# Kernel tuning notes

Hardware: AMD Instinct MI355X
Metric: run time of the kernel (lower is better)

## Reference

```python
import jax, jax.numpy as jnp
import numpy as np

N = 8192


def setup_inputs() -> dict:
    key = jax.random.key(0)
    k1, k2, k3 = jax.random.split(key, 3)
    # valid xyxy boxes: x1y1 in [0,1000), wh in (0,100]
    xy = jax.random.uniform(k1, (N, 2), dtype=jnp.float32) * 1000.0
    wh = jax.random.uniform(k2, (N, 2), dtype=jnp.float32) * 100.0 + 1.0
    boxes = jnp.concatenate([xy, xy + wh], axis=-1)  # [N,4]
    scores = jax.random.uniform(k3, (N,), dtype=jnp.float32)
    return {"boxes": boxes, "scores": scores, "iou_threshold": 0.5, "max_outputs": 100}


def _nms_keep_flags(boxes_sorted, iou_threshold):
    # boxes_sorted: [N,4] in descending-score order
    x1, y1, x2, y2 = (boxes_sorted[:, i] for i in range(4))
    areas = (x2 - x1) * (y2 - y1)  # [N]
    # pairwise intersection [N,N]
    iw = jnp.maximum(jnp.minimum(x2[:, None], x2[None, :]) - jnp.maximum(x1[:, None], x1[None, :]), 0.0)
    ih = jnp.maximum(jnp.minimum(y2[:, None], y2[None, :]) - jnp.maximum(y1[:, None], y1[None, :]), 0.0)
    inter = iw * ih
    iou = inter / (areas[:, None] + areas[None, :] - inter)
    sup = iou > iou_threshold  # [N,N]; diagonal True but handled below

    def body(suppressed, row):
        sup_row, i = row
        keep_i = jnp.logical_not(suppressed[i])
        suppressed = jnp.where(keep_i, suppressed | sup_row, suppressed)
        return suppressed, keep_i

    _, keep_flags = jax.lax.scan(
        body, jnp.zeros(sup.shape[0], dtype=bool), (sup, jnp.arange(sup.shape[0]))
    )
    return keep_flags  # [N] bool, in sorted order


def reference(boxes, scores, iou_threshold, max_outputs):
    n = scores.shape[0]
    order = jnp.argsort(-scores)  # descending, stable (matches torch sort tie-break)
    keep_flags = _nms_keep_flags(boxes[order], iou_threshold)
    # positions (in sorted order) of kept boxes; non-kept pushed to end
    pos = jnp.where(keep_flags, jnp.arange(n), n)
    pos = jnp.sort(pos)[:max_outputs]
    valid = pos < n
    idx = order[jnp.minimum(pos, n - 1)]
    # pad with -1 beyond the number of kept boxes (fixed-shape stand-in for keep[:max_outputs])
    return jnp.where(valid, idx, -1).astype(jnp.int32)
```

## Files before the change

kernel.cpp:

```cpp
#include <hip/hip_runtime.h>
#include <stdint.h>

#define THREADS 1024
#define NWAVE 16
#define NB 1024
#define NH 16
#define CAP 256
#define WANT 128
#define MAXKEEP 128
#define T0 0.9765625f

__device__ __forceinline__ float fence(float x) {
  asm("" : "+v"(x));
  return x;
}

__device__ __forceinline__ uint32_t rdlane32(uint32_t v, int l) {
  return (uint32_t)__builtin_amdgcn_readlane((int)v, l);
}

#define REGSTAGE(KK, JV)                                              \
  do {                                                                \
    _Pragma("unroll") for (int v = 0; v < 4; ++v) {                   \
      if ((v & (JV)) == 0) {                                          \
        uint64_t a = k[v], b = k[v | (JV)];                           \
        bool descRun = (((v * 64) & (KK)) == 0);                      \
        uint64_t mx = a > b ? a : b, mn = a > b ? b : a;              \
        k[v] = descRun ? mx : mn;                                     \
        k[v | (JV)] = descRun ? mn : mx;                              \
      }                                                               \
    }                                                                 \
  } while (0)

#define SHSTAGE(KK, J)                                                \
  do {                                                                \
    _Pragma("unroll") for (int v = 0; v < 4; ++v) {                   \
      uint64_t a = k[v];                                              \
      uint64_t b = __shfl_xor(a, (J), 64);                            \
      int e = v * 64 + lane;                                          \
      bool descRun = ((e & (KK)) == 0);                               \
      bool lower = ((lane & (J)) == 0);                               \
      uint64_t mx = a > b ? a : b, mn = a > b ? b : a;                \
      k[v] = (descRun == lower) ? mx : mn;                            \
    }                                                                 \
  } while (0)

#define SH32TO1(KK)                                                   \
  SHSTAGE(KK, 32); SHSTAGE(KK, 16); SHSTAGE(KK, 8);                   \
  SHSTAGE(KK, 4); SHSTAGE(KK, 2); SHSTAGE(KK, 1)

__device__ __forceinline__ void sort256(int lane, int cnt,
                                        const uint64_t* cand, uint64_t k[4]) {
#pragma unroll
  for (int v = 0; v < 4; ++v) {
    int e = v * 64 + lane;
    k[v] = (e < cnt) ? cand[e] : 0ull;
  }
  SHSTAGE(2, 1);
  SHSTAGE(4, 2); SHSTAGE(4, 1);
  SHSTAGE(8, 4); SHSTAGE(8, 2); SHSTAGE(8, 1);
  SHSTAGE(16, 8); SHSTAGE(16, 4); SHSTAGE(16, 2); SHSTAGE(16, 1);
  SHSTAGE(32, 16); SHSTAGE(32, 8); SHSTAGE(32, 4); SHSTAGE(32, 2);
  SHSTAGE(32, 1);
  SHSTAGE(64, 32); SHSTAGE(64, 16); SHSTAGE(64, 8); SHSTAGE(64, 4);
  SHSTAGE(64, 2); SHSTAGE(64, 1);
  REGSTAGE(128, 1); SH32TO1(128);
  REGSTAGE(256, 2); REGSTAGE(256, 1); SH32TO1(256);
}

__device__ __forceinline__ int greedy4(int lane, int cnt, int kept, int maxout,
                                       float thr, const uint64_t k[4],
                                       const float4* candbox, float4* cbox,
                                       float* careaS, float4* kbox,
                                       float* kareaS, int* kidxS) {
#pragma unroll
  for (int c = 0; c < 4; ++c) {
    if (c * 64 < cnt && kept < maxout) {
      uint64_t key = k[c];
      bool valid = (c * 64 + lane) < cnt;
      int slot = valid ? (int)(key & 0x3FFFF) : 0;
      int idx = valid ? (8192 - (int)((key >> 18) & 0x3FFF)) : 0;
      float4 bb = candbox[slot];
      float x1 = bb.x, y1 = bb.y, x2 = bb.z, y2 = bb.w;
      float areaj = fence((x2 - x1) * (y2 - y1));
      const int kbase = kept;

      bool supp = !valid;
#pragma unroll 4
      for (int t = 0; t < kbase; ++t) {
        float4 kb = kbox[t];
        float ka = kareaS[t];
        float iw = fmaxf(fminf(kb.z, x2) - fmaxf(kb.x, x1), 0.0f);
        float ih = fmaxf(fminf(kb.w, y2) - fmaxf(kb.y, y1), 0.0f);
        float inter = fence(iw * ih);
        float denom = (ka + areaj) - inter;
        if (inter / denom > thr) supp = true;
      }

      cbox[lane] = bb;
      careaS[lane] = areaj;
      uint64_t row = 0;
#pragma unroll 8
      for (int j = 0; j < 64; ++j) {
        float4 ib = cbox[j];
        float ia = careaS[j];
        float iw = fmaxf(fminf(ib.z, x2) - fmaxf(ib.x, x1), 0.0f);
        float ih = fmaxf(fminf(ib.w, y2) - fmaxf(ib.y, y1), 0.0f);
        float inter = fence(iw * ih);
        float denom = (ia + areaj) - inter;
        if (inter / denom > thr) row |= (1ull << j);
      }

      const uint64_t self = 1ull << lane;
      uint64_t alive = __ballot(valid && !supp);
      uint64_t rowNS = row & ~self;
      uint64_t conflict = __ballot(valid && !supp && ((rowNS & alive) != 0));
      uint64_t keepm;
      const int budget = maxout - kept;
      if (conflict == 0) {
        int na = __popcll((unsigned long long)alive);
        if (na <= budget) {
          keepm = alive;
          kept += na;
        } else {
          int lo = 0;
#pragma unroll
          for (int s = 32; s >= 1; s >>= 1) {
            int t2 = lo + s;
            uint64_t mk = (t2 >= 64) ? ~0ull : ((1ull << t2) - 1ull);
            if (__popcll((unsigned long long)(alive & mk)) < budget) lo = t2;
          }
          uint64_t mk2 = ((lo + 1) >= 64) ? ~0ull : ((1ull << (lo + 1)) - 1ull);
          keepm = alive & mk2;
          kept += budget;
        }
      } else {
        uint32_t rlo = (uint32_t)row, rhi = (uint32_t)(row >> 32);
        keepm = 0;
        while (alive != 0 && kept < maxout) {
          int b2 = __ffsll((unsigned long long)alive) - 1;
          keepm |= (1ull << b2);
          kept++;
          uint64_t rb = ((uint64_t)rdlane32(rhi, b2) << 32) |
                        (uint64_t)rdlane32(rlo, b2);
          alive &= ~rb;
          alive &= ~(1ull << b2);
        }
      }
      if ((keepm >> lane) & 1) {
        int rank = __popcll((unsigned long long)(keepm & (self - 1ull)));
        kbox[kbase + rank] = bb;
        kareaS[kbase + rank] = areaj;
        kidxS[kbase + rank] = idx;
      }
    }
  }
  return kept;
}

__global__ __launch_bounds__(THREADS) void nms_rank4_kernel(
    const float* __restrict__ boxes, const float* __restrict__ scores, int n,
    const float* __restrict__ thr_p, const int* __restrict__ maxout_p,
    int* __restrict__ out, int out_size) {
  __shared__ __align__(16) uint32_t hist[NH][NB];
  __shared__ uint32_t wcnt[NWAVE];
  __shared__ uint64_t cand[CAP];
  __shared__ float4 candbox[CAP];
  __shared__ float4 candboxR[CAP];
  __shared__ float2 cxyR[CAP];
  __shared__ float areaR[CAP];
  __shared__ int sidxR[CAP];
  __shared__ uint64_t adjm[CAP][4];
  __shared__ float4 cbox[64];
  __shared__ float careaS[64];
  __shared__ float4 kbox[MAXKEEP];
  __shared__ float kareaS[MAXKEEP];
  __shared__ int kidxS[MAXKEEP];
  __shared__ int s_cut, s_hi, s_kept, s_done;

  const int tid = threadIdx.x;
  const int lane = tid & 63;
  const int wid = tid >> 6;

  const float thr = *thr_p;
  int maxout = *maxout_p;
  if (maxout > out_size) maxout = out_size;
  if (maxout > MAXKEEP) maxout = MAXKEEP;

  float sc[8];
  const int base = tid * 8;
  if (base + 7 < n) {
    const float4* sp = reinterpret_cast<const float4*>(scores) + 2 * tid;
    float4 a = sp[0], b2 = sp[1];
    sc[0] = a.x; sc[1] = a.y; sc[2] = a.z; sc[3] = a.w;
    sc[4] = b2.x; sc[5] = b2.y; sc[6] = b2.z; sc[7] = b2.w;
  } else {
#pragma unroll
    for (int r = 0; r < 8; ++r)
      sc[r] = (base + r < n) ? scores[base + r] : -1.0f;
  }

  int wtot = 0;
#pragma unroll
  for (int r = 0; r < 8; ++r) {
    bool pred = (base + r < n) && (sc[r] >= T0);
    wtot += __popcll((unsigned long long)__ballot(pred));
  }
  if (lane == 0) wcnt[wid] = (uint32_t)wtot;
  __syncthreads();
  int cbase = 0, total = 0;
#pragma unroll
  for (int w = 0; w < NWAVE; ++w) {
    int c = (int)wcnt[w];
    if (w < wid) cbase += c;
    total += c;
  }

  const bool fast_ok = (total <= CAP);
  bool done = false;
  if (fast_ok) {
    int run = cbase;
#pragma unroll
    for (int r = 0; r < 8; ++r) {
      int idx = base + r;
      bool pred = (idx < n) && (sc[r] >= T0);
      uint64_t m = __ballot(pred);
      if (pred) {
        int pos = run + __popcll((unsigned long long)(m & ((1ull << lane) - 1)));
        cand[pos] = ((uint64_t)__float_as_uint(sc[r]) << 32) |
                    ((uint64_t)(8192 - idx) << 18) | (uint64_t)pos;
      }
      run += __popcll((unsigned long long)m);
    }
    if (tid >= total && tid < CAP) cand[tid] = 0;
    __syncthreads();

    const int cnt = total;
    const int c = tid >> 2;
    const int h = tid & 3;

    uint64_t mykey = 0;
    float4 bb;
    int myidx = 0;
    if (c < cnt) {
      mykey = cand[c];
      if (h == 0) {
        myidx = 8192 - (int)((mykey >> 18) & 0x3FFF);
        bb = *reinterpret_cast<const float4*>(boxes + 4 * (size_t)myidx);
      }
    }

    int rc = 0;
    {
      int r0 = 0, r1 = 0;
#pragma unroll
      for (int i = 0; i < CAP / 8; ++i) {
        uint64_t ka = cand[8 * i + h];
        uint64_t kb = cand[8 * i + 4 + h];
        r0 += (ka > mykey) ? 1 : 0;
        r1 += (kb > mykey) ? 1 : 0;
      }
      rc = r0 + r1;
    }
    rc += __shfl_xor(rc, 1, 64);
    rc += __shfl_xor(rc, 2, 64);
    if (c < cnt && h == 0) {
      candboxR[rc] = bb;
      sidxR[rc] = myidx;
      cxyR[rc] = make_float2((bb.x + bb.z) * 0.5f, (bb.y + bb.w) * 0.5f);
      areaR[rc] = fence((bb.z - bb.x) * (bb.w - bb.y));
    }
    __syncthreads();

    if (c < cnt) {
      float4 mb = candboxR[c];
      float marea = areaR[c];
      float mcx = (mb.x + mb.z) * 0.5f;
      float mcy = (mb.y + mb.w) * 0.5f;
      float mrx = (mb.z - mb.x) * 0.5f;
      float mry = (mb.w - mb.y) * 0.5f;
      const bool use_pf = (thr >= 0.0f);
      uint64_t acc = 0;
      const int qbase = h << 6;
#pragma unroll
      for (int j = 0; j < 64; ++j) {
        const int q = qbase + j;
        if (q < cnt) {
          float2 cq = cxyR[q];
          float2 eq = make_float2(candboxR[q].z - candboxR[q].x,
                                  candboxR[q].w - candboxR[q].y);
          float dx = fabsf(cq.x - mcx);
          float dy = fabsf(cq.y - mcy);
          bool close = !use_pf | ((dx * 2.0f <= (mrx * 2.0f + eq.x) * 1.0000002f) &
                                  (dy * 2.0f <= (mry * 2.0f + eq.y) * 1.0000002f));
          if (close) {
            float4 qb = candboxR[q];
            float qarea = areaR[q];
            float iw = fmaxf(fminf(qb.z, mb.z) - fmaxf(qb.x, mb.x), 0.0f);
            float ih = fmaxf(fminf(qb.w, mb.w) - fmaxf(qb.y, mb.y), 0.0f);
            float inter = fence(iw * ih);
            float denom = (qarea + marea) - inter;
            if (inter / denom > thr) acc |= (1ull << j);
          }
        }
      }
      adjm[c][h] = acc;
    }
    __syncthreads();

    if (wid == 0) {
      uint64_t km[4] = {0, 0, 0, 0};
      int kept = 0;
#pragma unroll
      for (int cch = 0; cch < 4; ++cch) {
        if (cch * 64 < cnt && kept < maxout) {
          const int p = cch * 64 + lane;
          const bool valid = p < cnt;
          uint64_t r0 = 0, r1 = 0, r2 = 0, r3 = 0;
          if (valid) {
            r0 = adjm[p][0]; r1 = adjm[p][1];
            r2 = adjm[p][2]; r3 = adjm[p][3];
          }
          const uint64_t self = 1ull << lane;
          bool supp = !valid ||
                      (((r0 & km[0]) | (r1 & km[1]) | (r2 & km[2]) |
                        (r3 & km[3])) != 0);
          uint64_t alive = __ballot(valid && !supp);
          uint64_t wc = (cch == 0) ? r0 : (cch == 1) ? r1 : (cch == 2) ? r2 : r3;
          uint64_t conflict =
              __ballot(valid && !supp && ((wc & ~self & alive) != 0));
          uint64_t keepm;
          const int kbase = kept;
          const int budget = maxout - kept;
          if (conflict == 0) {
            int na = __popcll((unsigned long long)alive);
            if (na <= budget) {
              keepm = alive;
              kept += na;
            } else {
              int lo = 0;
#pragma unroll
              for (int s = 32; s >= 1; s >>= 1) {
                int t2 = lo + s;
                uint64_t mk = (t2 >= 64) ? ~0ull : ((1ull << t2) - 1ull);
                if (__popcll((unsigned long long)(alive & mk)) < budget) lo = t2;
              }
              uint64_t mk2 =
                  ((lo + 1) >= 64) ? ~0ull : ((1ull << (lo + 1)) - 1ull);
              keepm = alive & mk2;
              kept += budget;
            }
          } else {
            uint32_t rlo = (uint32_t)wc, rhi = (uint32_t)(wc >> 32);
            keepm = 0;
            while (alive != 0 && kept < maxout) {
              int b2 = __ffsll((unsigned long long)alive) - 1;
              keepm |= (1ull << b2);
              kept++;
              uint64_t rb = ((uint64_t)rdlane32(rhi, b2) << 32) |
                            (uint64_t)rdlane32(rlo, b2);
              alive &= ~rb;
              alive &= ~(1ull << b2);
            }
          }
          km[cch] = keepm;
          if ((keepm >> lane) & 1) {
            int rk = kbase +
                     __popcll((unsigned long long)(keepm & (self - 1ull)));
            kidxS[rk] = sidxR[p];
            float4 pb = candboxR[p];
            kbox[rk] = pb;
            kareaS[rk] = fence((pb.z - pb.x) * (pb.w - pb.y));
          }
        }
      }
      if (lane == 0) {
        s_kept = kept;
        s_done = (kept >= maxout) ? 1 : 0;
      }
    }
    __syncthreads();
    done = (s_done != 0);
  }

  if (!done) {
    {
      uint32_t* hh = &hist[0][0];
      for (int i = tid; i < NH * NB; i += THREADS) hh[i] = 0;
    }
    if (tid == 0) {
      s_hi = fast_ok ? 999 : (NB - 1);
      if (!fast_ok) s_kept = 0;
      s_done = 0;
    }
    __syncthreads();
    const int hicap = fast_ok ? 999 : (NB - 1);
    {
      uint32_t* myh = hist[wid];
#pragma unroll
      for (int r = 0; r < 8; ++r) {
        if (base + r < n) {
          int b = (int)(sc[r] * (float)NB);
          b = b < 0 ? 0 : (b > NB - 1 ? NB - 1 : b);
          if (b <= hicap) atomicAdd(&myh[b], 1u);
        }
      }
    }
    __syncthreads();
    for (int i = tid; i < NB; i += THREADS) {
      uint32_t s = 0;
#pragma unroll
      for (int hh = 0; hh < NH; ++hh) s += hist[hh][i];
      hist[0][i] = s;
    }
    __syncthreads();

    while (true) {
      if (wid == 0) {
        uint32_t csum = 0;
        const uint4* hp = reinterpret_cast<const uint4*>(&hist[0][lane * 16]);
#pragma unroll
        for (int i = 0; i < 4; ++i) {
          uint4 h4 = hp[i];
          csum += h4.x + h4.y + h4.z + h4.w;
        }
        uint32_t suf = csum;
#pragma unroll
        for (int off = 1; off < 64; off <<= 1) {
          uint32_t v = __shfl_down(suf, off, 64);
          suf += (lane + off < 64) ? v : 0u;
        }
        uint64_t mask = __ballot(suf >= (uint32_t)WANT);
        int cut;
        if (mask == 0) {
          cut = 0;
        } else {
          int cstar = 63 - __builtin_clzll((unsigned long long)mask);
          int src = cstar + 1 < 63 ? cstar + 1 : 63;
          uint32_t above_raw = __shfl(suf, src, 64);
          uint32_t above = (cstar < 63) ? above_raw : 0u;
          uint32_t h2 = (lane < 16) ? hist[0][cstar * 16 + lane] : 0u;
          uint32_t suf2 = h2;
#pragma unroll
          for (int off = 1; off < 64; off <<= 1) {
            uint32_t v = __shfl_down(suf2, off, 64);
            suf2 += (lane + off < 64) ? v : 0u;
          }
          uint64_t mask2 =
              __ballot((lane < 16) && (above + suf2 >= (uint32_t)WANT));
          int b2 = 63 - __builtin_clzll((unsigned long long)mask2);
          cut = cstar * 16 + b2;
        }
        if (lane == 0) s_cut = cut;
      }
      __syncthreads();
      const int cut = s_cut;
      const int hi = s_hi;
      const float lo_f =
          (cut == 0) ? -__builtin_huge_valf() : (float)cut / (float)NB;
      const bool top_open = (hi == NB - 1);
      const float up_f = (float)(hi + 1) / (float)NB;

      int wt = 0;
#pragma unroll
      for (int r = 0; r < 8; ++r) {
        int idx = base + r;
        bool pred = (idx < n) && (sc[r] >= lo_f) && (top_open || sc[r] < up_f);
        wt += __popcll((unsigned long long)__ballot(pred));
      }
      if (lane == 0) wcnt[wid] = (uint32_t)wt;
      __syncthreads();
      int cb2 = 0, tot2 = 0;
#pragma unroll
      for (int w = 0; w < NWAVE; ++w) {
        int cc = (int)wcnt[w];
        if (w < wid) cb2 += cc;
        tot2 += cc;
      }
      {
        int run2 = cb2;
#pragma unroll
        for (int r = 0; r < 8; ++r) {
          int idx = base + r;
          bool pred =
              (idx < n) && (sc[r] >= lo_f) && (top_open || sc[r] < up_f);
          uint64_t m = __ballot(pred);
          if (pred) {
            int pos =
                run2 + __popcll((unsigned long long)(m & ((1ull << lane) - 1)));
            if (pos < CAP) {
              cand[pos] = ((uint64_t)__float_as_uint(sc[r]) << 32) |
                          ((uint64_t)(8192 - idx) << 18) | (uint64_t)pos;
              candbox[pos] =
                  *reinterpret_cast<const float4*>(boxes + 4 * (size_t)idx);
            }
          }
          run2 += __popcll((unsigned long long)m);
        }
      }
      __syncthreads();
      int cnt2 = tot2 > CAP ? CAP : tot2;
      if (wid == 0) {
        uint64_t k2[4];
        sort256(lane, cnt2, cand, k2);
        int kept = greedy4(lane, cnt2, s_kept, maxout, thr, k2, candbox, cbox,
                           careaS, kbox, kareaS, kidxS);
        if (lane == 0) {
          s_kept = kept;
          s_hi = cut - 1;
          s_done = (kept >= maxout || cut == 0) ? 1 : 0;
        }
      }
      __syncthreads();
      if (s_done) break;
      for (int b = cut + tid; b <= hi; b += THREADS) hist[0][b] = 0;
      __syncthreads();
    }
  }

  const int keptf = s_kept;
  for (int i = tid; i < out_size; i += THREADS)
    out[i] = (i < keptf) ? kidxS[i] : -1;
}

extern "C" void kernel_launch(void* const* d_in, const int* in_sizes, int n_in,
                              void* d_out, int out_size, void* d_ws,
                              size_t ws_size, hipStream_t stream) {
  const float* boxes = (const float*)d_in[0];
  const float* scores = (const float*)d_in[1];
  const float* thr = (const float*)d_in[2];
  const int* maxout = (const int*)d_in[3];
  int n = in_sizes[1];
  int* out = (int*)d_out;

  hipLaunchKernelGGL(nms_rank4_kernel, dim3(1), dim3(THREADS), 0, stream,
                     boxes, scores, n, thr, maxout, out, out_size);
}
```

Baseline: 26.16 us.

## Redistribute IoU rows across threads, use max-radius prefilter, batch greedy conflict resolution

Remaps the adjacency computation so each thread handles one (candidate, 64-column chunk) pair by tid&255 and tid>>8, skipping chunks beyond the candidate count. It replaces the per-pair proximity test with a cheaper bound built from a block-wide max half-extent reduced through shuffles and an LDS atomicMax. The greedy pass now keeps whole conflict-free runs at once and only falls back to one step per conflicting lane, then trims to the output budget. Wave 0 also writes the output directly and the block returns early, so the final global store is skipped. This adds a reduction, an atomic and a looser prefilter that may admit more exact IoU checks.

```diff
diff --git a/kernel.cpp b/kernel.cpp
--- a/kernel.cpp
+++ b/kernel.cpp
@@ -158,7 +158,7 @@
   return kept;
 }
 
-__global__ __launch_bounds__(THREADS) void nms_rank4_kernel(
+__global__ __launch_bounds__(THREADS) void nms_rank5_kernel(
     const float* __restrict__ boxes, const float* __restrict__ scores, int n,
     const float* __restrict__ thr_p, const int* __restrict__ maxout_p,
     int* __restrict__ out, int out_size) {
@@ -176,7 +176,7 @@
   __shared__ float4 kbox[MAXKEEP];
   __shared__ float kareaS[MAXKEEP];
   __shared__ int kidxS[MAXKEEP];
-  __shared__ int s_cut, s_hi, s_kept, s_done;
+  __shared__ int s_cut, s_hi, s_kept, s_done, s_rmax_i;
 
   const int tid = threadIdx.x;
   const int lane = tid & 63;
@@ -207,6 +207,7 @@
     wtot += __popcll((unsigned long long)__ballot(pred));
   }
   if (lane == 0) wcnt[wid] = (uint32_t)wtot;
+  if (tid == 0) s_rmax_i = 0;
   __syncthreads();
   int cbase = 0, total = 0;
 #pragma unroll
@@ -264,6 +265,15 @@
     }
     rc += __shfl_xor(rc, 1, 64);
     rc += __shfl_xor(rc, 2, 64);
+
+    float rm = 0.0f;
+    if (c < cnt && h == 0)
+      rm = fmaxf((bb.z - bb.x) * 0.5f, (bb.w - bb.y) * 0.5f);
+#pragma unroll
+    for (int off = 1; off < 64; off <<= 1)
+      rm = fmaxf(rm, __shfl_xor(rm, off, 64));
+    if (lane == 0) atomicMax(&s_rmax_i, __float_as_int(rm));
+
     if (c < cnt && h == 0) {
       candboxR[rc] = bb;
       sidxR[rc] = myidx;
@@ -272,39 +282,45 @@
     }
     __syncthreads();
 
-    if (c < cnt) {
-      float4 mb = candboxR[c];
-      float marea = areaR[c];
-      float mcx = (mb.x + mb.z) * 0.5f;
-      float mcy = (mb.y + mb.w) * 0.5f;
-      float mrx = (mb.z - mb.x) * 0.5f;
-      float mry = (mb.w - mb.y) * 0.5f;
-      const bool use_pf = (thr >= 0.0f);
-      uint64_t acc = 0;
-      const int qbase = h << 6;
-#pragma unroll
-      for (int j = 0; j < 64; ++j) {
-        const int q = qbase + j;
-        if (q < cnt) {
-          float2 cq = cxyR[q];
-          float2 eq = make_float2(candboxR[q].z - candboxR[q].x,
-                                  candboxR[q].w - candboxR[q].y);
-          float dx = fabsf(cq.x - mcx);
-          float dy = fabsf(cq.y - mcy);
-          bool close = !use_pf | ((dx * 2.0f <= (mrx * 2.0f + eq.x) * 1.0000002f) &
-                                  (dy * 2.0f <= (mry * 2.0f + eq.y) * 1.0000002f));
-          if (close) {
-            float4 qb = candboxR[q];
-            float qarea = areaR[q];
-            float iw = fmaxf(fminf(qb.z, mb.z) - fmaxf(qb.x, mb.x), 0.0f);
-            float ih = fmaxf(fminf(qb.w, mb.w) - fmaxf(qb.y, mb.y), 0.0f);
-            float inter = fence(iw * ih);
-            float denom = (qarea + marea) - inter;
-            if (inter / denom > thr) acc |= (1ull << j);
-          }
-        }
-      }
-      adjm[c][h] = acc;
+    {
+      const int c2 = tid & 255;
+      const int h2 = tid >> 8;
+      const int qbase = h2 << 6;
+      if (c2 < cnt) {
+        uint64_t acc = 0;
+        if (qbase < cnt) {
+          float4 mb = candboxR[c2];
+          float marea = areaR[c2];
+          float mcx = (mb.x + mb.z) * 0.5f;
+          float mcy = (mb.y + mb.w) * 0.5f;
+          float mrx = (mb.z - mb.x) * 0.5f;
+          float mry = (mb.w - mb.y) * 0.5f;
+          const float rmaxf = __int_as_float(s_rmax_i);
+          const float limx = mrx + rmaxf + 0.002f;
+          const float limy = mry + rmaxf + 0.002f;
+          const bool use_pf = (thr >= 0.0f);
+#pragma unroll
+          for (int j = 0; j < 64; ++j) {
+            const int q = qbase + j;
+            if (q < cnt) {
+              float2 cq = cxyR[q];
+              bool close = (fabsf(cq.x - mcx) <= limx) &
+                           (fabsf(cq.y - mcy) <= limy);
+              if (!use_pf) close = true;
+              if (close) {
+                float4 qb = candboxR[q];
+                float qarea = areaR[q];
+                float iw = fmaxf(fminf(qb.z, mb.z) - fmaxf(qb.x, mb.x), 0.0f);
+                float ih = fmaxf(fminf(qb.w, mb.w) - fmaxf(qb.y, mb.y), 0.0f);
+                float inter = fence(iw * ih);
+                float denom = (qarea + marea) - inter;
+                if (inter / denom > thr) acc |= (1ull << j);
+              }
+            }
+          }
+        }
+        adjm[c2][h2] = acc;
+      }
     }
     __syncthreads();
 
@@ -327,43 +343,40 @@
                         (r3 & km[3])) != 0);
           uint64_t alive = __ballot(valid && !supp);
           uint64_t wc = (cch == 0) ? r0 : (cch == 1) ? r1 : (cch == 2) ? r2 : r3;
-          uint64_t conflict =
-              __ballot(valid && !supp && ((wc & ~self & alive) != 0));
-          uint64_t keepm;
+          uint64_t rowNS = wc & ~self;
+          uint32_t rlo = (uint32_t)wc, rhi = (uint32_t)(wc >> 32);
+          uint64_t keepm = 0;
+          while (alive != 0) {
+            bool ma = (alive >> lane) & 1;
+            uint64_t conf = __ballot(ma && ((rowNS & alive) != 0));
+            if (conf == 0) {
+              keepm |= alive;
+              break;
+            }
+            int cb = __ffsll((unsigned long long)conf) - 1;
+            uint64_t incl = (cb >= 63) ? ~0ull : ((1ull << (cb + 1)) - 1ull);
+            keepm |= alive & incl;
+            alive &= ~incl;
+            uint64_t rb = ((uint64_t)rdlane32(rhi, cb) << 32) |
+                          (uint64_t)rdlane32(rlo, cb);
+            alive &= ~rb;
+          }
+          int nk = __popcll((unsigned long long)keepm);
+          const int budget = maxout - kept;
+          if (nk > budget) {
+            int lo = 0;
+#pragma unroll
+            for (int s = 32; s >= 1; s >>= 1) {
+              int t2 = lo + s;
+              uint64_t mk = (t2 >= 64) ? ~0ull : ((1ull << t2) - 1ull);
+              if (__popcll((unsigned long long)(keepm & mk)) < budget) lo = t2;
+            }
+            keepm &= (lo >= 63) ? ~0ull : ((1ull << (lo + 1)) - 1ull);
+            nk = budget;
+          }
+          km[cch] = keepm;
           const int kbase = kept;
-          const int budget = maxout - kept;
-          if (conflict == 0) {
-            int na = __popcll((unsigned long long)alive);
-            if (na <= budget) {
-              keepm = alive;
-              kept += na;
-            } else {
-              int lo = 0;
-#pragma unroll
-              for (int s = 32; s >= 1; s >>= 1) {
-                int t2 = lo + s;
-                uint64_t mk = (t2 >= 64) ? ~0ull : ((1ull << t2) - 1ull);
-                if (__popcll((unsigned long long)(alive & mk)) < budget) lo = t2;
-              }
-              uint64_t mk2 =
-                  ((lo + 1) >= 64) ? ~0ull : ((1ull << (lo + 1)) - 1ull);
-              keepm = alive & mk2;
-              kept += budget;
-            }
-          } else {
-            uint32_t rlo = (uint32_t)wc, rhi = (uint32_t)(wc >> 32);
-            keepm = 0;
-            while (alive != 0 && kept < maxout) {
-              int b2 = __ffsll((unsigned long long)alive) - 1;
-              keepm |= (1ull << b2);
-              kept++;
-              uint64_t rb = ((uint64_t)rdlane32(rhi, b2) << 32) |
-                            (uint64_t)rdlane32(rlo, b2);
-              alive &= ~rb;
-              alive &= ~(1ull << b2);
-            }
-          }
-          km[cch] = keepm;
+          kept += nk;
           if ((keepm >> lane) & 1) {
             int rk = kbase +
                      __popcll((unsigned long long)(keepm & (self - 1ull)));
@@ -374,6 +387,8 @@
           }
         }
       }
+      for (int i = lane; i < out_size; i += 64)
+        out[i] = (i < kept) ? kidxS[i] : -1;
       if (lane == 0) {
         s_kept = kept;
         s_done = (kept >= maxout) ? 1 : 0;
@@ -381,9 +396,10 @@
     }
     __syncthreads();
     done = (s_done != 0);
-  }
-
-  if (!done) {
+    if (done) return;
+  }
+
+  {
     {
       uint32_t* hh = &hist[0][0];
       for (int i = tid; i < NH * NB; i += THREADS) hh[i] = 0;
@@ -533,6 +549,6 @@
   int n = in_sizes[1];
   int* out = (int*)d_out;
 
-  hipLaunchKernelGGL(nms_rank4_kernel, dim3(1), dim3(THREADS), 0, stream,
+  hipLaunchKernelGGL(nms_rank5_kernel, dim3(1), dim3(THREADS), 0, stream,
                      boxes, scores, n, thr, maxout, out, out_size);
 }
```

New measurement: 23.25 us. -11.1%, faster.
